# Performance work log

Hardware: AMD Instinct MI355X
Metric: run time of the kernel (lower is better)

The kernel has to match this reference:

```python
import jax, jax.numpy as jnp
import numpy as np

ALPHA = 0.05
KSIZE = 7
SIGMA = 7.0  # SecondMomentMatrixLayer calls get_gaussian_kernel(ksize, ksize)


def _gaussian_kernel(ksize, sigma):
    ax = np.arange(ksize, dtype=np.float32) - (ksize - 1) / 2.0
    g1 = np.exp(-(ax ** 2) / (2.0 * sigma ** 2))
    g2 = np.outer(g1, g1)
    g2 = g2 / g2.sum()
    return jnp.asarray(g2, dtype=jnp.float32)


def setup_inputs() -> dict:
    key = jax.random.key(0)
    x = jax.random.uniform(key, (1, 1, 2048, 4096), dtype=jnp.float32)
    # Sobel filters (cross-correlation weights, as torch conv2d uses)
    wx = jnp.array([[-1., 0., 1.], [-2., 0., 2.], [-1., 0., 1.]], dtype=jnp.float32)
    wy = wx.T
    sobel_w = jnp.stack([wx, wy], axis=0)[:, None]  # (2,1,3,3)
    gauss_w = _gaussian_kernel(KSIZE, SIGMA)[None, None]  # (1,1,7,7)
    return {"x": x, "sobel_w": sobel_w, "gauss_w": gauss_w}


def _conv_same(x, w, groups=1):
    # x: (N,C,H,W), w: (O,C/g,kh,kw); torch-style cross-correlation, SAME padding
    return jax.lax.conv_general_dilated(
        x, w, window_strides=(1, 1), padding="SAME",
        dimension_numbers=("NCHW", "OIHW", "NCHW"),
        feature_group_count=groups)


def reference(x, sobel_w, gauss_w):
    # 1) image gradients: (N,1,H,W) -> (N,2,H,W)
    g = _conv_same(x, sobel_w)
    ix, iy = g[:, 0], g[:, 1]  # (N,H,W)
    # 2) channel products Ixx, Iyy, Ixy: (N,3,H,W)
    prod = jnp.stack([ix * ix, iy * iy, ix * iy], axis=1)
    # 3) Gaussian smoothing of each channel (same kernel depthwise)
    gw3 = jnp.broadcast_to(gauss_w, (3, 1, KSIZE, KSIZE))
    s = _conv_same(prod, gw3, groups=3)
    sxx, syy, sxy = s[:, 0], s[:, 1], s[:, 2]  # (N,H,W)
    # 4) corner response R = det - alpha*trace^2 (with the original's extra unsqueeze(0))
    r = (sxx * syy - sxy * sxy) - ALPHA * ((sxx + syy) ** 2)[None]  # (1,N,H,W) -> (1,1,H,W) for N=1
    # 5) NMS: threshold at (lower) median, 7x7 stride-1 maxpool, equality mask, multiply
    flat = r.ravel()
    k = (flat.shape[0] - 1) // 2  # torch.median -> lower median
    med = jnp.partition(flat, k)[k]
    thr = jnp.where(r > med, r, jnp.float32(0))
    pooled = jax.lax.reduce_window(
        thr, -jnp.inf, jax.lax.max, (1, 1, KSIZE, KSIZE), (1, 1, 1, 1), "SAME")
    mask = jnp.where(pooled == thr, jnp.float32(1), jnp.float32(0))
    return mask * r
```

## Files before the change

kernel.cpp:

```cpp
#include <hip/hip_runtime.h>
#include <hip/hip_bf16.h>
#include <math.h>

#define H 2048
#define W 4096
#define NPIX (H * W)
#define KSEL 4194303u
#define NT 512
#define TSX 64
#define TSY 32
#define NBX (W / TSX)
#define NBY (H / TSY)

__device__ __forceinline__ unsigned fmap(float f) {
    unsigned u = __float_as_uint(f);
    return (u & 0x80000000u) ? ~u : (u | 0x80000000u);
}
__device__ __forceinline__ float4 ld4s(const float* p) { return *(const float4*)p; }
__device__ __forceinline__ void st4s(float* p, float4 v) { *(float4*)p = v; }

#define SMF 13480
#define SXA(r,c) smem[5472 + (r)*76 + (c)]
#define GXA(r,c) smem[(r)*72 + (c)]
#define GYA(r,c) smem[2736 + (r)*72 + (c)]
#define H0A(r,c) smem[5472 + (r)*68 + (c)]
#define H1A(r,c) smem[8056 + (r)*68 + (c)]
#define H2A(r,c) smem[10640 + (r)*68 + (c)]

__global__ __launch_bounds__(NT) void k_response(const float* __restrict__ x,
                                                 const float* __restrict__ gw,
                                                 float* __restrict__ r,
                                                 unsigned* __restrict__ hist1) {
    __shared__ float smem[SMF];
    unsigned* lh = (unsigned*)&smem[13224];

    int tl = threadIdx.x;
    int bx = blockIdx.x & (NBX - 1);
    int by = blockIdx.x >> 6;
    int tx0 = bx * TSX, ty0 = by * TSY;

    float hwr[7], vwr[7];
    float g33 = gw[24];
#pragma unroll
    for (int b = 0; b < 7; ++b) hwr[b] = gw[21 + b];
#pragma unroll
    for (int a = 0; a < 7; ++a) vwr[a] = gw[a * 7 + 3] / g33;

    if (tl < 256) lh[tl] = 0;

#pragma unroll
    for (int it = 0; it < 2; ++it) {
        int task = tl + it * NT;
        if (task < 720) {
            int row = task / 18, g = task - row * 18;
            int gy = ty0 - 4 + row;
            int gx0 = tx0 - 4 + 4 * g;
            float4 v = make_float4(0.f, 0.f, 0.f, 0.f);
            if ((unsigned)gy < H) {
                if ((unsigned)gx0 <= (unsigned)(W - 4)) {
                    v = *(const float4*)&x[(size_t)gy * W + gx0];
                } else {
                    float* vv = (float*)&v;
#pragma unroll
                    for (int k = 0; k < 4; ++k) {
                        int c = gx0 + k;
                        if ((unsigned)c < W) vv[k] = x[(size_t)gy * W + c];
                    }
                }
            }
            st4s(&SXA(row, 4 * g), v);
        }
    }
    __syncthreads();

#pragma unroll
    for (int it = 0; it < 2; ++it) {
        int task = tl + it * NT;
        if (task < 684) {
            int row = task / 18, g = task - row * 18;
            int base = 4 * g;
            float w0[8], w1[8], w2[8];
            {
                float4 t0 = ld4s(&SXA(row, base)), t1 = ld4s(&SXA(row, base + 4));
                w0[0]=t0.x; w0[1]=t0.y; w0[2]=t0.z; w0[3]=t0.w; w0[4]=t1.x; w0[5]=t1.y; w0[6]=t1.z; w0[7]=t1.w;
                t0 = ld4s(&SXA(row + 1, base)); t1 = ld4s(&SXA(row + 1, base + 4));
                w1[0]=t0.x; w1[1]=t0.y; w1[2]=t0.z; w1[3]=t0.w; w1[4]=t1.x; w1[5]=t1.y; w1[6]=t1.z; w1[7]=t1.w;
                t0 = ld4s(&SXA(row + 2, base)); t1 = ld4s(&SXA(row + 2, base + 4));
                w2[0]=t0.x; w2[1]=t0.y; w2[2]=t0.z; w2[3]=t0.w; w2[4]=t1.x; w2[5]=t1.y; w2[6]=t1.z; w2[7]=t1.w;
            }
            int rowOK = ((unsigned)(ty0 - 3 + row) < H);
            float4 gxv, gyv;
            float* pgx = (float*)&gxv;
            float* pgy = (float*)&gyv;
#pragma unroll
            for (int k = 0; k < 4; ++k) {
                float ixv = (w0[k + 2] - w0[k]) + 2.f * (w1[k + 2] - w1[k]) + (w2[k + 2] - w2[k]);
                float iyv = (w2[k] - w0[k]) + 2.f * (w2[k + 1] - w0[k + 1]) + (w2[k + 2] - w0[k + 2]);
                int gc = tx0 + base + k - 3;
                bool ok = rowOK && ((unsigned)gc < W);
                pgx[k] = ok ? ixv : 0.f;
                pgy[k] = ok ? iyv : 0.f;
            }
            st4s(&GXA(row, base), gxv);
            st4s(&GYA(row, base), gyv);
        }
    }
    __syncthreads();

#pragma unroll
    for (int it = 0; it < 2; ++it) {
        int task = tl + it * NT;
        if (task < 608) {
            int row = task >> 4, c0 = (task & 15) * 4;
            float wgx[12], wgy[12];
            {
                float4 t0 = ld4s(&GXA(row, c0)), t1 = ld4s(&GXA(row, c0 + 4)), t2 = ld4s(&GXA(row, c0 + 8));
                wgx[0]=t0.x; wgx[1]=t0.y; wgx[2]=t0.z; wgx[3]=t0.w; wgx[4]=t1.x; wgx[5]=t1.y; wgx[6]=t1.z; wgx[7]=t1.w;
                wgx[8]=t2.x; wgx[9]=t2.y; wgx[10]=t2.z; wgx[11]=t2.w;
                t0 = ld4s(&GYA(row, c0)); t1 = ld4s(&GYA(row, c0 + 4)); t2 = ld4s(&GYA(row, c0 + 8));
                wgy[0]=t0.x; wgy[1]=t0.y; wgy[2]=t0.z; wgy[3]=t0.w; wgy[4]=t1.x; wgy[5]=t1.y; wgy[6]=t1.z; wgy[7]=t1.w;
                wgy[8]=t2.x; wgy[9]=t2.y; wgy[10]=t2.z; wgy[11]=t2.w;
            }
            float px[10], py[10], pxy[10];
#pragma unroll
            for (int i = 0; i < 10; ++i) {
                px[i] = wgx[i] * wgx[i];
                py[i] = wgy[i] * wgy[i];
                pxy[i] = wgx[i] * wgy[i];
            }
            float4 s0, s1, s2;
            float* q0 = (float*)&s0; float* q1 = (float*)&s1; float* q2 = (float*)&s2;
#pragma unroll
            for (int k = 0; k < 4; ++k) {
                float a0 = 0.f, a1 = 0.f, a2 = 0.f;
#pragma unroll
                for (int b = 0; b < 7; ++b) {
                    float w = hwr[b];
                    a0 += w * px[k + b];
                    a1 += w * py[k + b];
                    a2 += w * pxy[k + b];
                }
                q0[k] = a0; q1[k] = a1; q2[k] = a2;
            }
            st4s(&H0A(row, c0), s0);
            st4s(&H1A(row, c0), s1);
            st4s(&H2A(row, c0), s2);
        }
    }
    __syncthreads();

    {
        int ii = tl >> 4, c0 = (tl & 15) * 4;
        float4 a0 = make_float4(0.f, 0.f, 0.f, 0.f), a1 = a0, a2 = a0;
#pragma unroll
        for (int a = 0; a < 7; ++a) {
            float w = vwr[a];
            float4 h0v = ld4s(&H0A(ii + a, c0));
            float4 h1v = ld4s(&H1A(ii + a, c0));
            float4 h2v = ld4s(&H2A(ii + a, c0));
            a0.x += w * h0v.x; a0.y += w * h0v.y; a0.z += w * h0v.z; a0.w += w * h0v.w;
            a1.x += w * h1v.x; a1.y += w * h1v.y; a1.z += w * h1v.z; a1.w += w * h1v.w;
            a2.x += w * h2v.x; a2.y += w * h2v.y; a2.z += w * h2v.z; a2.w += w * h2v.w;
        }
        float* sxx = (float*)&a0; float* syy = (float*)&a1; float* sxy = (float*)&a2;
        float4 rv4;
        float* prv = (float*)&rv4;
#pragma unroll
        for (int k = 0; k < 4; ++k) {
            float tr = sxx[k] + syy[k];
            float rv = sxx[k] * syy[k] - sxy[k] * sxy[k] - 0.05f * tr * tr;
            prv[k] = rv;
        }
        st4s(&r[(size_t)(ty0 + ii) * W + tx0 + c0], rv4);
#pragma unroll
        for (int k = 0; k < 4; ++k) atomicAdd(&lh[fmap(prv[k]) >> 24], 1u);
    }
    __syncthreads();
    if (tl < 256 && lh[tl]) atomicAdd(&hist1[tl], lh[tl]);
}

__global__ __launch_bounds__(256) void k_scan256(const unsigned* __restrict__ hist,
                                                 unsigned* __restrict__ sel,
                                                 int in_rank_idx, int out_base) {
    __shared__ unsigned s[256];
    int t = threadIdx.x;
    unsigned c = hist[t];
    s[t] = c;
    __syncthreads();
    for (int off = 1; off < 256; off <<= 1) {
        unsigned v = (t >= off) ? s[t - off] : 0u;
        __syncthreads();
        s[t] += v;
        __syncthreads();
    }
    unsigned k = (in_rank_idx < 0) ? KSEL : sel[in_rank_idx];
    unsigned cumb = s[t] - c;
    if (k >= cumb && k < s[t]) {
        sel[out_base] = (unsigned)t;
        sel[out_base + 1] = k - cumb;
    }
}

__global__ __launch_bounds__(256) void k_hist2(const float* __restrict__ r,
                                               const unsigned* __restrict__ sel,
                                               unsigned* __restrict__ hist2) {
    __shared__ unsigned lh[256];
    lh[threadIdx.x] = 0;
    __syncthreads();
    unsigned b1 = sel[0];
    int idx = blockIdx.x * blockDim.x + threadIdx.x;
    int stride = gridDim.x * blockDim.x;
    const float4* r4 = (const float4*)r;
    for (int i = idx; i < NPIX / 4; i += stride) {
        float4 v = r4[i];
        unsigned u;
        u = fmap(v.x); if ((u >> 24) == b1) atomicAdd(&lh[(u >> 16) & 0xFF], 1u);
        u = fmap(v.y); if ((u >> 24) == b1) atomicAdd(&lh[(u >> 16) & 0xFF], 1u);
        u = fmap(v.z); if ((u >> 24) == b1) atomicAdd(&lh[(u >> 16) & 0xFF], 1u);
        u = fmap(v.w); if ((u >> 24) == b1) atomicAdd(&lh[(u >> 16) & 0xFF], 1u);
    }
    __syncthreads();
    if (lh[threadIdx.x]) atomicAdd(&hist2[threadIdx.x], lh[threadIdx.x]);
}

__global__ __launch_bounds__(256) void k_hist3(const float* __restrict__ r,
                                               const unsigned* __restrict__ sel,
                                               unsigned* __restrict__ hist3) {
    unsigned top16 = (sel[0] << 8) | sel[2];
    int idx = blockIdx.x * blockDim.x + threadIdx.x;
    int stride = gridDim.x * blockDim.x;
    const float4* r4 = (const float4*)r;
    for (int i = idx; i < NPIX / 4; i += stride) {
        float4 v = r4[i];
        unsigned u;
        u = fmap(v.x); if ((u >> 16) == top16) atomicAdd(&hist3[u & 0xFFFF], 1u);
        u = fmap(v.y); if ((u >> 16) == top16) atomicAdd(&hist3[u & 0xFFFF], 1u);
        u = fmap(v.z); if ((u >> 16) == top16) atomicAdd(&hist3[u & 0xFFFF], 1u);
        u = fmap(v.w); if ((u >> 16) == top16) atomicAdd(&hist3[u & 0xFFFF], 1u);
    }
}

__global__ __launch_bounds__(256) void k_scan64k(const unsigned* __restrict__ hist3,
                                                 unsigned* __restrict__ sel) {
    __shared__ unsigned s[256];
    int t = threadIdx.x;
    unsigned sum = 0;
    for (int i = 0; i < 256; ++i) sum += hist3[t * 256 + i];
    s[t] = sum;
    __syncthreads();
    for (int off = 1; off < 256; off <<= 1) {
        unsigned v = (t >= off) ? s[t - off] : 0u;
        __syncthreads();
        s[t] += v;
        __syncthreads();
    }
    unsigned k = sel[3];
    unsigned cumb = s[t] - sum;
    if (k >= cumb && k < s[t]) {
        unsigned rem = k - cumb;
        unsigned cum = 0, b3 = 0;
        for (int i = 0; i < 256; ++i) {
            unsigned c = hist3[t * 256 + i];
            if (rem < cum + c) { b3 = (unsigned)(t * 256 + i); break; }
            cum += c;
        }
        unsigned med_u = (sel[0] << 24) | (sel[2] << 16) | b3;
        unsigned bits = (med_u & 0x80000000u) ? (med_u & 0x7FFFFFFFu) : ~med_u;
        ((float*)sel)[4] = __uint_as_float(bits);
    }
}

#define RTA(r,c) smem[(r)*76 + (c)]
#define THA(r,c) smem[2888 + (r)*76 + (c)]
#define HMA(r,c) smem[5776 + (r)*68 + (c)]

__global__ __launch_bounds__(NT) void k_final(const float* __restrict__ r,
                                              const unsigned* __restrict__ sel,
                                              float* __restrict__ out) {
    __shared__ float smem[8360];
    float med = ((const float*)sel)[4];
    int tl = threadIdx.x;
    int bx = blockIdx.x & (NBX - 1);
    int by = blockIdx.x >> 6;
    int tx0 = bx * TSX, ty0 = by * TSY;
    const float NINF = -INFINITY;

#pragma unroll
    for (int it = 0; it < 2; ++it) {
        int task = tl + it * NT;
        if (task < 684) {
            int row = task / 18, g = task - row * 18;
            int gy = ty0 - 3 + row;
            int gx0 = tx0 - 4 + 4 * g;
            float4 v = make_float4(NINF, NINF, NINF, NINF);
            float4 tv = v;
            float* pv = (float*)&v; float* ptv = (float*)&tv;
            if ((unsigned)gy < H) {
                if ((unsigned)gx0 <= (unsigned)(W - 4)) {
                    v = *(const float4*)&r[(size_t)gy * W + gx0];
#pragma unroll
                    for (int k = 0; k < 4; ++k) ptv[k] = (pv[k] > med) ? pv[k] : 0.f;
                } else {
#pragma unroll
                    for (int k = 0; k < 4; ++k) {
                        int c = gx0 + k;
                        if ((unsigned)c < W) {
                            float rv = r[(size_t)gy * W + c];
                            pv[k] = rv;
                            ptv[k] = (rv > med) ? rv : 0.f;
                        }
                    }
                }
            }
            st4s(&RTA(row, 4 * g), v);
            st4s(&THA(row, 4 * g), tv);
        }
    }
    __syncthreads();

#pragma unroll
    for (int it = 0; it < 2; ++it) {
        int task = tl + it * NT;
        if (task < 608) {
            int row = task >> 4, c0 = (task & 15) * 4;
            float w[12];
            {
                float4 t0 = ld4s(&THA(row, c0)), t1 = ld4s(&THA(row, c0 + 4)), t2 = ld4s(&THA(row, c0 + 8));
                w[0]=t0.x; w[1]=t0.y; w[2]=t0.z; w[3]=t0.w; w[4]=t1.x; w[5]=t1.y; w[6]=t1.z; w[7]=t1.w;
                w[8]=t2.x; w[9]=t2.y; w[10]=t2.z; w[11]=t2.w;
            }
            float4 m4;
            float* pm = (float*)&m4;
#pragma unroll
            for (int k = 0; k < 4; ++k) {
                float m = w[k + 1];
#pragma unroll
                for (int b = 2; b < 8; ++b) m = fmaxf(m, w[k + b]);
                pm[k] = m;
            }
            st4s(&HMA(row, c0), m4);
        }
    }
    __syncthreads();

    {
        int ii = tl >> 4, c0 = (tl & 15) * 4;
        float4 m = ld4s(&HMA(ii, c0));
#pragma unroll
        for (int a = 1; a < 7; ++a) {
            float4 h = ld4s(&HMA(ii + a, c0));
            m.x = fmaxf(m.x, h.x); m.y = fmaxf(m.y, h.y);
            m.z = fmaxf(m.z, h.z); m.w = fmaxf(m.w, h.w);
        }
        float4 rv = ld4s(&RTA(ii + 3, c0 + 4));
        float4 tv = ld4s(&THA(ii + 3, c0 + 4));
        float4 o;
        o.x = (m.x == tv.x) ? rv.x : 0.f;
        o.y = (m.y == tv.y) ? rv.y : 0.f;
        o.z = (m.z == tv.z) ? rv.z : 0.f;
        o.w = (m.w == tv.w) ? rv.w : 0.f;
        st4s(&out[(size_t)(ty0 + ii) * W + tx0 + c0], o);
    }
}

extern "C" void kernel_launch(void* const* d_in, const int* in_sizes, int n_in,
                              void* d_out, int out_size, void* d_ws, size_t ws_size,
                              hipStream_t stream) {
    const float* x = (const float*)d_in[0];
    const float* gw = (const float*)d_in[2];
    float* out = (float*)d_out;

    char* ws = (char*)d_ws;
    float* r = (float*)ws;
    unsigned* hist1 = (unsigned*)(ws + (size_t)NPIX * 4);
    unsigned* hist2 = hist1 + 256;
    unsigned* hist3 = hist2 + 256;
    unsigned* sel = hist3 + 65536;

    hipMemsetAsync(hist1, 0, (256 + 256 + 65536 + 8) * sizeof(unsigned), stream);

    int nblk = NBX * NBY;
    k_response<<<nblk, NT, 0, stream>>>(x, gw, r, hist1);
    k_scan256<<<1, 256, 0, stream>>>(hist1, sel, -1, 0);
    k_hist2<<<1024, 256, 0, stream>>>(r, sel, hist2);
    k_scan256<<<1, 256, 0, stream>>>(hist2, sel, 1, 2);
    k_hist3<<<1024, 256, 0, stream>>>(r, sel, hist3);
    k_scan64k<<<1, 256, 0, stream>>>(hist3, sel);
    k_final<<<nblk, NT, 0, stream>>>(r, sel, out);
}
```

Measured before the change: 140.7 us.

## Fold scan kernels into histogram kernels via last-block ticket; fuse Sobel into products

Removes the three single-block scan launches by having the last block of each histogram kernel, found with an atomic ticket counter, do the prefix scan and bucket selection. In k_response, the Sobel gradient stage is merged into the horizontal Gaussian stage, which drops one shared-memory pass, one barrier and the gradient buffers, and the block now requests higher occupancy. k_final stops staging a separate thresholded tile and recomputes the threshold from the raw response in registers, halving its shared-memory footprint. In exchange the Sobel values are recomputed for overlapping columns, and the kernels now rely on cross-block atomic ordering.

```diff
diff --git a/kernel.cpp b/kernel.cpp
--- a/kernel.cpp
+++ b/kernel.cpp
@@ -18,21 +18,30 @@
 }
 __device__ __forceinline__ float4 ld4s(const float* p) { return *(const float4*)p; }
 __device__ __forceinline__ void st4s(float* p, float4 v) { *(float4*)p = v; }
-
-#define SMF 13480
-#define SXA(r,c) smem[5472 + (r)*76 + (c)]
-#define GXA(r,c) smem[(r)*72 + (c)]
-#define GYA(r,c) smem[2736 + (r)*72 + (c)]
-#define H0A(r,c) smem[5472 + (r)*68 + (c)]
-#define H1A(r,c) smem[8056 + (r)*68 + (c)]
-#define H2A(r,c) smem[10640 + (r)*68 + (c)]
-
-__global__ __launch_bounds__(NT) void k_response(const float* __restrict__ x,
-                                                 const float* __restrict__ gw,
-                                                 float* __restrict__ r,
-                                                 unsigned* __restrict__ hist1) {
-    __shared__ float smem[SMF];
-    unsigned* lh = (unsigned*)&smem[13224];
+__device__ __forceinline__ void ld12(const float* p, float* d) {
+    float4 a = ld4s(p), b = ld4s(p + 4), c = ld4s(p + 8);
+    d[0]=a.x; d[1]=a.y; d[2]=a.z; d[3]=a.w;
+    d[4]=b.x; d[5]=b.y; d[6]=b.z; d[7]=b.w;
+    d[8]=c.x; d[9]=c.y; d[10]=c.z; d[11]=c.w;
+}
+__device__ __forceinline__ unsigned aload(const unsigned* p) {
+    return __hip_atomic_load(p, __ATOMIC_RELAXED, __HIP_MEMORY_SCOPE_AGENT);
+}
+
+#define SX(r,c) smem[(r)*72 + (c)]
+#define H0(r,c) smem[2880 + (r)*64 + (c)]
+#define H1(r,c) smem[5312 + (r)*64 + (c)]
+#define H2(r,c) smem[7744 + (r)*64 + (c)]
+
+__global__ __launch_bounds__(NT, 8) void k_response(const float* __restrict__ x,
+                                                    const float* __restrict__ gw,
+                                                    float* __restrict__ r,
+                                                    unsigned* __restrict__ hist1,
+                                                    unsigned* __restrict__ sel,
+                                                    unsigned* __restrict__ tick) {
+    __shared__ float smem[10176];
+    __shared__ unsigned lastf;
+    unsigned* lh = (unsigned*)smem;
 
     int tl = threadIdx.x;
     int bx = blockIdx.x & (NBX - 1);
@@ -45,8 +54,6 @@
     for (int b = 0; b < 7; ++b) hwr[b] = gw[21 + b];
 #pragma unroll
     for (int a = 0; a < 7; ++a) vwr[a] = gw[a * 7 + 3] / g33;
-
-    if (tl < 256) lh[tl] = 0;
 
 #pragma unroll
     for (int it = 0; it < 2; ++it) {
@@ -68,41 +75,7 @@
                     }
                 }
             }
-            st4s(&SXA(row, 4 * g), v);
-        }
-    }
-    __syncthreads();
-
-#pragma unroll
-    for (int it = 0; it < 2; ++it) {
-        int task = tl + it * NT;
-        if (task < 684) {
-            int row = task / 18, g = task - row * 18;
-            int base = 4 * g;
-            float w0[8], w1[8], w2[8];
-            {
-                float4 t0 = ld4s(&SXA(row, base)), t1 = ld4s(&SXA(row, base + 4));
-                w0[0]=t0.x; w0[1]=t0.y; w0[2]=t0.z; w0[3]=t0.w; w0[4]=t1.x; w0[5]=t1.y; w0[6]=t1.z; w0[7]=t1.w;
-                t0 = ld4s(&SXA(row + 1, base)); t1 = ld4s(&SXA(row + 1, base + 4));
-                w1[0]=t0.x; w1[1]=t0.y; w1[2]=t0.z; w1[3]=t0.w; w1[4]=t1.x; w1[5]=t1.y; w1[6]=t1.z; w1[7]=t1.w;
-                t0 = ld4s(&SXA(row + 2, base)); t1 = ld4s(&SXA(row + 2, base + 4));
-                w2[0]=t0.x; w2[1]=t0.y; w2[2]=t0.z; w2[3]=t0.w; w2[4]=t1.x; w2[5]=t1.y; w2[6]=t1.z; w2[7]=t1.w;
-            }
-            int rowOK = ((unsigned)(ty0 - 3 + row) < H);
-            float4 gxv, gyv;
-            float* pgx = (float*)&gxv;
-            float* pgy = (float*)&gyv;
-#pragma unroll
-            for (int k = 0; k < 4; ++k) {
-                float ixv = (w0[k + 2] - w0[k]) + 2.f * (w1[k + 2] - w1[k]) + (w2[k + 2] - w2[k]);
-                float iyv = (w2[k] - w0[k]) + 2.f * (w2[k + 1] - w0[k + 1]) + (w2[k + 2] - w0[k + 2]);
-                int gc = tx0 + base + k - 3;
-                bool ok = rowOK && ((unsigned)gc < W);
-                pgx[k] = ok ? ixv : 0.f;
-                pgy[k] = ok ? iyv : 0.f;
-            }
-            st4s(&GXA(row, base), gxv);
-            st4s(&GYA(row, base), gyv);
+            st4s(&SX(row, 4 * g), v);
         }
     }
     __syncthreads();
@@ -111,23 +84,37 @@
     for (int it = 0; it < 2; ++it) {
         int task = tl + it * NT;
         if (task < 608) {
-            int row = task >> 4, c0 = (task & 15) * 4;
-            float wgx[12], wgy[12];
-            {
-                float4 t0 = ld4s(&GXA(row, c0)), t1 = ld4s(&GXA(row, c0 + 4)), t2 = ld4s(&GXA(row, c0 + 8));
-                wgx[0]=t0.x; wgx[1]=t0.y; wgx[2]=t0.z; wgx[3]=t0.w; wgx[4]=t1.x; wgx[5]=t1.y; wgx[6]=t1.z; wgx[7]=t1.w;
-                wgx[8]=t2.x; wgx[9]=t2.y; wgx[10]=t2.z; wgx[11]=t2.w;
-                t0 = ld4s(&GYA(row, c0)); t1 = ld4s(&GYA(row, c0 + 4)); t2 = ld4s(&GYA(row, c0 + 8));
-                wgy[0]=t0.x; wgy[1]=t0.y; wgy[2]=t0.z; wgy[3]=t0.w; wgy[4]=t1.x; wgy[5]=t1.y; wgy[6]=t1.z; wgy[7]=t1.w;
-                wgy[8]=t2.x; wgy[9]=t2.y; wgy[10]=t2.z; wgy[11]=t2.w;
-            }
+            int gr = task >> 4;
+            int c0 = (task & 15) << 2;
+            int rowOK = ((unsigned)(ty0 - 3 + gr) < H);
+            int xbase = tx0 + c0 - 3;
+
+            float x0[12], x1[12], x2[12];
+            ld12(&SX(gr, c0), x0);
+            ld12(&SX(gr + 1, c0), x1);
+            ld12(&SX(gr + 2, c0), x2);
+
+            float hd0[10], hd1[10], hd2[10], d[12];
+#pragma unroll
+            for (int p = 0; p < 10; ++p) hd0[p] = x0[p + 2] - x0[p];
+#pragma unroll
+            for (int p = 0; p < 10; ++p) hd1[p] = x1[p + 2] - x1[p];
+#pragma unroll
+            for (int p = 0; p < 10; ++p) hd2[p] = x2[p + 2] - x2[p];
+#pragma unroll
+            for (int p = 0; p < 12; ++p) d[p] = x2[p] - x0[p];
+
             float px[10], py[10], pxy[10];
 #pragma unroll
-            for (int i = 0; i < 10; ++i) {
-                px[i] = wgx[i] * wgx[i];
-                py[i] = wgy[i] * wgy[i];
-                pxy[i] = wgx[i] * wgy[i];
-            }
+            for (int p = 0; p < 10; ++p) {
+                float ix = hd0[p] + 2.f * hd1[p] + hd2[p];
+                float iy = d[p] + 2.f * d[p + 1] + d[p + 2];
+                bool ok = rowOK && ((unsigned)(xbase + p) < W);
+                float gxv = ok ? ix : 0.f;
+                float gyv = ok ? iy : 0.f;
+                px[p] = gxv * gxv; py[p] = gyv * gyv; pxy[p] = gxv * gyv;
+            }
+
             float4 s0, s1, s2;
             float* q0 = (float*)&s0; float* q1 = (float*)&s1; float* q2 = (float*)&s2;
 #pragma unroll
@@ -142,22 +129,25 @@
                 }
                 q0[k] = a0; q1[k] = a1; q2[k] = a2;
             }
-            st4s(&H0A(row, c0), s0);
-            st4s(&H1A(row, c0), s1);
-            st4s(&H2A(row, c0), s2);
-        }
-    }
+            st4s(&H0(gr, c0), s0);
+            st4s(&H1(gr, c0), s1);
+            st4s(&H2(gr, c0), s2);
+        }
+    }
+    __syncthreads();
+
+    if (tl < 256) lh[tl] = 0;
     __syncthreads();
 
     {
-        int ii = tl >> 4, c0 = (tl & 15) * 4;
+        int ii = tl >> 4, c0 = (tl & 15) << 2;
         float4 a0 = make_float4(0.f, 0.f, 0.f, 0.f), a1 = a0, a2 = a0;
 #pragma unroll
         for (int a = 0; a < 7; ++a) {
             float w = vwr[a];
-            float4 h0v = ld4s(&H0A(ii + a, c0));
-            float4 h1v = ld4s(&H1A(ii + a, c0));
-            float4 h2v = ld4s(&H2A(ii + a, c0));
+            float4 h0v = ld4s(&H0(ii + a, c0));
+            float4 h1v = ld4s(&H1(ii + a, c0));
+            float4 h2v = ld4s(&H2(ii + a, c0));
             a0.x += w * h0v.x; a0.y += w * h0v.y; a0.z += w * h0v.z; a0.w += w * h0v.w;
             a1.x += w * h1v.x; a1.y += w * h1v.y; a1.z += w * h1v.z; a1.w += w * h1v.w;
             a2.x += w * h2v.x; a2.y += w * h2v.y; a2.z += w * h2v.z; a2.w += w * h2v.w;
@@ -168,47 +158,51 @@
 #pragma unroll
         for (int k = 0; k < 4; ++k) {
             float tr = sxx[k] + syy[k];
-            float rv = sxx[k] * syy[k] - sxy[k] * sxy[k] - 0.05f * tr * tr;
-            prv[k] = rv;
+            prv[k] = sxx[k] * syy[k] - sxy[k] * sxy[k] - 0.05f * tr * tr;
         }
         st4s(&r[(size_t)(ty0 + ii) * W + tx0 + c0], rv4);
 #pragma unroll
         for (int k = 0; k < 4; ++k) atomicAdd(&lh[fmap(prv[k]) >> 24], 1u);
     }
     __syncthreads();
+
     if (tl < 256 && lh[tl]) atomicAdd(&hist1[tl], lh[tl]);
-}
-
-__global__ __launch_bounds__(256) void k_scan256(const unsigned* __restrict__ hist,
-                                                 unsigned* __restrict__ sel,
-                                                 int in_rank_idx, int out_base) {
-    __shared__ unsigned s[256];
+    __syncthreads();
+
+    if (tl == 0)
+        lastf = (__hip_atomic_fetch_add(tick, 1u, __ATOMIC_ACQ_REL, __HIP_MEMORY_SCOPE_AGENT)
+                 == (unsigned)(gridDim.x - 1)) ? 1u : 0u;
+    __syncthreads();
+    if (lastf) {
+        unsigned* ss = (unsigned*)(smem + 256);
+        unsigned c = 0;
+        if (tl < 256) { c = aload(&hist1[tl]); ss[tl] = c; }
+        __syncthreads();
+        for (int off = 1; off < 256; off <<= 1) {
+            unsigned v = 0;
+            if (tl >= off && tl < 256) v = ss[tl - off];
+            __syncthreads();
+            if (tl < 256) ss[tl] += v;
+            __syncthreads();
+        }
+        if (tl < 256) {
+            unsigned inc = ss[tl], cumb = inc - c;
+            if (KSEL >= cumb && KSEL < inc) { sel[0] = (unsigned)tl; sel[1] = KSEL - cumb; }
+        }
+    }
+}
+
+__global__ __launch_bounds__(256) void k_hist2(const float* __restrict__ r,
+                                               unsigned* __restrict__ sel,
+                                               unsigned* __restrict__ hist2,
+                                               unsigned* __restrict__ tick) {
+    __shared__ unsigned lh[256];
+    __shared__ unsigned lastf;
     int t = threadIdx.x;
-    unsigned c = hist[t];
-    s[t] = c;
-    __syncthreads();
-    for (int off = 1; off < 256; off <<= 1) {
-        unsigned v = (t >= off) ? s[t - off] : 0u;
-        __syncthreads();
-        s[t] += v;
-        __syncthreads();
-    }
-    unsigned k = (in_rank_idx < 0) ? KSEL : sel[in_rank_idx];
-    unsigned cumb = s[t] - c;
-    if (k >= cumb && k < s[t]) {
-        sel[out_base] = (unsigned)t;
-        sel[out_base + 1] = k - cumb;
-    }
-}
-
-__global__ __launch_bounds__(256) void k_hist2(const float* __restrict__ r,
-                                               const unsigned* __restrict__ sel,
-                                               unsigned* __restrict__ hist2) {
-    __shared__ unsigned lh[256];
-    lh[threadIdx.x] = 0;
+    lh[t] = 0;
     __syncthreads();
     unsigned b1 = sel[0];
-    int idx = blockIdx.x * blockDim.x + threadIdx.x;
+    int idx = blockIdx.x * blockDim.x + t;
     int stride = gridDim.x * blockDim.x;
     const float4* r4 = (const float4*)r;
     for (int i = idx; i < NPIX / 4; i += stride) {
@@ -220,14 +214,37 @@
         u = fmap(v.w); if ((u >> 24) == b1) atomicAdd(&lh[(u >> 16) & 0xFF], 1u);
     }
     __syncthreads();
-    if (lh[threadIdx.x]) atomicAdd(&hist2[threadIdx.x], lh[threadIdx.x]);
+    if (lh[t]) atomicAdd(&hist2[t], lh[t]);
+    __syncthreads();
+    if (t == 0)
+        lastf = (__hip_atomic_fetch_add(tick, 1u, __ATOMIC_ACQ_REL, __HIP_MEMORY_SCOPE_AGENT)
+                 == (unsigned)(gridDim.x - 1)) ? 1u : 0u;
+    __syncthreads();
+    if (lastf) {
+        unsigned c = aload(&hist2[t]);
+        lh[t] = c;
+        __syncthreads();
+        for (int off = 1; off < 256; off <<= 1) {
+            unsigned v = (t >= off) ? lh[t - off] : 0u;
+            __syncthreads();
+            lh[t] += v;
+            __syncthreads();
+        }
+        unsigned k = sel[1];
+        unsigned cumb = lh[t] - c;
+        if (k >= cumb && k < lh[t]) { sel[2] = (unsigned)t; sel[3] = k - cumb; }
+    }
 }
 
 __global__ __launch_bounds__(256) void k_hist3(const float* __restrict__ r,
-                                               const unsigned* __restrict__ sel,
-                                               unsigned* __restrict__ hist3) {
+                                               unsigned* __restrict__ sel,
+                                               unsigned* __restrict__ hist3,
+                                               unsigned* __restrict__ tick) {
+    __shared__ unsigned ss[256];
+    __shared__ unsigned lastf;
+    int t = threadIdx.x;
     unsigned top16 = (sel[0] << 8) | sel[2];
-    int idx = blockIdx.x * blockDim.x + threadIdx.x;
+    int idx = blockIdx.x * blockDim.x + t;
     int stride = gridDim.x * blockDim.x;
     const float4* r4 = (const float4*)r;
     for (int i = idx; i < NPIX / 4; i += stride) {
@@ -238,46 +255,46 @@
         u = fmap(v.z); if ((u >> 16) == top16) atomicAdd(&hist3[u & 0xFFFF], 1u);
         u = fmap(v.w); if ((u >> 16) == top16) atomicAdd(&hist3[u & 0xFFFF], 1u);
     }
-}
-
-__global__ __launch_bounds__(256) void k_scan64k(const unsigned* __restrict__ hist3,
-                                                 unsigned* __restrict__ sel) {
-    __shared__ unsigned s[256];
-    int t = threadIdx.x;
-    unsigned sum = 0;
-    for (int i = 0; i < 256; ++i) sum += hist3[t * 256 + i];
-    s[t] = sum;
-    __syncthreads();
-    for (int off = 1; off < 256; off <<= 1) {
-        unsigned v = (t >= off) ? s[t - off] : 0u;
+    __syncthreads();
+    if (t == 0)
+        lastf = (__hip_atomic_fetch_add(tick, 1u, __ATOMIC_ACQ_REL, __HIP_MEMORY_SCOPE_AGENT)
+                 == (unsigned)(gridDim.x - 1)) ? 1u : 0u;
+    __syncthreads();
+    if (lastf) {
+        unsigned sum = 0;
+        for (int i = 0; i < 256; ++i) sum += aload(&hist3[t * 256 + i]);
+        ss[t] = sum;
         __syncthreads();
-        s[t] += v;
-        __syncthreads();
-    }
-    unsigned k = sel[3];
-    unsigned cumb = s[t] - sum;
-    if (k >= cumb && k < s[t]) {
-        unsigned rem = k - cumb;
-        unsigned cum = 0, b3 = 0;
-        for (int i = 0; i < 256; ++i) {
-            unsigned c = hist3[t * 256 + i];
-            if (rem < cum + c) { b3 = (unsigned)(t * 256 + i); break; }
-            cum += c;
-        }
-        unsigned med_u = (sel[0] << 24) | (sel[2] << 16) | b3;
-        unsigned bits = (med_u & 0x80000000u) ? (med_u & 0x7FFFFFFFu) : ~med_u;
-        ((float*)sel)[4] = __uint_as_float(bits);
-    }
-}
-
-#define RTA(r,c) smem[(r)*76 + (c)]
-#define THA(r,c) smem[2888 + (r)*76 + (c)]
-#define HMA(r,c) smem[5776 + (r)*68 + (c)]
+        for (int off = 1; off < 256; off <<= 1) {
+            unsigned v = (t >= off) ? ss[t - off] : 0u;
+            __syncthreads();
+            ss[t] += v;
+            __syncthreads();
+        }
+        unsigned k = sel[3];
+        unsigned cumb = ss[t] - sum;
+        if (k >= cumb && k < ss[t]) {
+            unsigned rem = k - cumb;
+            unsigned cum = 0, b3 = 0;
+            for (int i = 0; i < 256; ++i) {
+                unsigned c = aload(&hist3[t * 256 + i]);
+                if (rem < cum + c) { b3 = (unsigned)(t * 256 + i); break; }
+                cum += c;
+            }
+            unsigned med_u = (sel[0] << 24) | (sel[2] << 16) | b3;
+            unsigned bits = (med_u & 0x80000000u) ? (med_u & 0x7FFFFFFFu) : ~med_u;
+            ((float*)sel)[4] = __uint_as_float(bits);
+        }
+    }
+}
+
+#define RT(r,c) smem[(r)*72 + (c)]
+#define HM(r,c) smem[2736 + (r)*64 + (c)]
 
 __global__ __launch_bounds__(NT) void k_final(const float* __restrict__ r,
                                               const unsigned* __restrict__ sel,
                                               float* __restrict__ out) {
-    __shared__ float smem[8360];
+    __shared__ float smem[5168];
     float med = ((const float*)sel)[4];
     int tl = threadIdx.x;
     int bx = blockIdx.x & (NBX - 1);
@@ -293,27 +310,19 @@
             int gy = ty0 - 3 + row;
             int gx0 = tx0 - 4 + 4 * g;
             float4 v = make_float4(NINF, NINF, NINF, NINF);
-            float4 tv = v;
-            float* pv = (float*)&v; float* ptv = (float*)&tv;
             if ((unsigned)gy < H) {
                 if ((unsigned)gx0 <= (unsigned)(W - 4)) {
                     v = *(const float4*)&r[(size_t)gy * W + gx0];
-#pragma unroll
-                    for (int k = 0; k < 4; ++k) ptv[k] = (pv[k] > med) ? pv[k] : 0.f;
                 } else {
+                    float* pv = (float*)&v;
 #pragma unroll
                     for (int k = 0; k < 4; ++k) {
                         int c = gx0 + k;
-                        if ((unsigned)c < W) {
-                            float rv = r[(size_t)gy * W + c];
-                            pv[k] = rv;
-                            ptv[k] = (rv > med) ? rv : 0.f;
-                        }
+                        if ((unsigned)c < W) pv[k] = r[(size_t)gy * W + c];
                     }
                 }
             }
-            st4s(&RTA(row, 4 * g), v);
-            st4s(&THA(row, 4 * g), tv);
+            st4s(&RT(row, 4 * g), v);
         }
     }
     __syncthreads();
@@ -322,43 +331,48 @@
     for (int it = 0; it < 2; ++it) {
         int task = tl + it * NT;
         if (task < 608) {
-            int row = task >> 4, c0 = (task & 15) * 4;
+            int row = task >> 4, c0 = (task & 15) << 2;
             float w[12];
-            {
-                float4 t0 = ld4s(&THA(row, c0)), t1 = ld4s(&THA(row, c0 + 4)), t2 = ld4s(&THA(row, c0 + 8));
-                w[0]=t0.x; w[1]=t0.y; w[2]=t0.z; w[3]=t0.w; w[4]=t1.x; w[5]=t1.y; w[6]=t1.z; w[7]=t1.w;
-                w[8]=t2.x; w[9]=t2.y; w[10]=t2.z; w[11]=t2.w;
+            ld12(&RT(row, c0), w);
+            float th[11];
+#pragma unroll
+            for (int j = 1; j <= 10; ++j) {
+                float v = w[j];
+                th[j] = (v > med) ? v : ((v == NINF) ? NINF : 0.f);
             }
             float4 m4;
             float* pm = (float*)&m4;
 #pragma unroll
             for (int k = 0; k < 4; ++k) {
-                float m = w[k + 1];
-#pragma unroll
-                for (int b = 2; b < 8; ++b) m = fmaxf(m, w[k + b]);
+                float m = th[k + 1];
+#pragma unroll
+                for (int b = 2; b < 8; ++b) m = fmaxf(m, th[k + b]);
                 pm[k] = m;
             }
-            st4s(&HMA(row, c0), m4);
+            st4s(&HM(row, c0), m4);
         }
     }
     __syncthreads();
 
     {
-        int ii = tl >> 4, c0 = (tl & 15) * 4;
-        float4 m = ld4s(&HMA(ii, c0));
+        int ii = tl >> 4, c0 = (tl & 15) << 2;
+        float4 m = ld4s(&HM(ii, c0));
 #pragma unroll
         for (int a = 1; a < 7; ++a) {
-            float4 h = ld4s(&HMA(ii + a, c0));
+            float4 h = ld4s(&HM(ii + a, c0));
             m.x = fmaxf(m.x, h.x); m.y = fmaxf(m.y, h.y);
             m.z = fmaxf(m.z, h.z); m.w = fmaxf(m.w, h.w);
         }
-        float4 rv = ld4s(&RTA(ii + 3, c0 + 4));
-        float4 tv = ld4s(&THA(ii + 3, c0 + 4));
+        float4 rv = ld4s(&RT(ii + 3, c0 + 4));
         float4 o;
-        o.x = (m.x == tv.x) ? rv.x : 0.f;
-        o.y = (m.y == tv.y) ? rv.y : 0.f;
-        o.z = (m.z == tv.z) ? rv.z : 0.f;
-        o.w = (m.w == tv.w) ? rv.w : 0.f;
+        float tvx = (rv.x > med) ? rv.x : 0.f;
+        float tvy = (rv.y > med) ? rv.y : 0.f;
+        float tvz = (rv.z > med) ? rv.z : 0.f;
+        float tvw = (rv.w > med) ? rv.w : 0.f;
+        o.x = (m.x == tvx) ? rv.x : 0.f;
+        o.y = (m.y == tvy) ? rv.y : 0.f;
+        o.z = (m.z == tvz) ? rv.z : 0.f;
+        o.w = (m.w == tvw) ? rv.w : 0.f;
         st4s(&out[(size_t)(ty0 + ii) * W + tx0 + c0], o);
     }
 }
@@ -376,15 +390,13 @@
     unsigned* hist2 = hist1 + 256;
     unsigned* hist3 = hist2 + 256;
     unsigned* sel = hist3 + 65536;
-
-    hipMemsetAsync(hist1, 0, (256 + 256 + 65536 + 8) * sizeof(unsigned), stream);
+    unsigned* tick = sel + 8;
+
+    hipMemsetAsync(hist1, 0, (256 + 256 + 65536 + 8 + 4) * sizeof(unsigned), stream);
 
     int nblk = NBX * NBY;
-    k_response<<<nblk, NT, 0, stream>>>(x, gw, r, hist1);
-    k_scan256<<<1, 256, 0, stream>>>(hist1, sel, -1, 0);
-    k_hist2<<<1024, 256, 0, stream>>>(r, sel, hist2);
-    k_scan256<<<1, 256, 0, stream>>>(hist2, sel, 1, 2);
-    k_hist3<<<1024, 256, 0, stream>>>(r, sel, hist3);
-    k_scan64k<<<1, 256, 0, stream>>>(hist3, sel);
+    k_response<<<nblk, NT, 0, stream>>>(x, gw, r, hist1, sel, tick);
+    k_hist2<<<1024, 256, 0, stream>>>(r, sel, hist2, tick + 1);
+    k_hist3<<<1024, 256, 0, stream>>>(r, sel, hist3, tick + 2);
     k_final<<<nblk, NT, 0, stream>>>(r, sel, out);
 }
```

New measurement: 273.5 us. 1.94x slower.
